# Kernel tuning notes

Measured on AMD Instinct MI355X. Metric: run time of the kernel, lower is better.

The kernel has to match this reference:

```python
import jax, jax.numpy as jnp
import numpy as np


def cheb_mats(N: int, degree: int):
    """Analysis/synthesis Chebyshev matrices, matching torch reference.
    Returns T_pinv [d+1, N], T_eval [N, d+1] as float32 jnp arrays."""
    x = np.linspace(0.0, 1.0, N, dtype=np.float32)
    xn = np.clip(2.0 * x - 1.0, -1 + 1e-06, 1 - 1e-06)
    theta = np.arccos(xn)
    ks = np.arange(degree + 1, dtype=np.float32)
    T = np.cos(theta[:, None] * ks[None, :])  # [N, d+1]
    T_pinv = np.linalg.pinv(T.astype(np.float64)).astype(np.float32)  # [d+1, N]
    return jnp.asarray(T_pinv), jnp.asarray(T.astype(np.float32))


def setup_inputs() -> dict:
    key = jax.random.key(0)
    k1, k2, k3 = jax.random.split(key, 3)
    B, C, H, W = 32, 64, 128, 128
    out_ch, degree = 64, 8
    scale_w = (2.0 / (C * (degree + 1))) ** 0.5
    scale_h = (2.0 / (out_ch * (degree + 1))) ** 0.5
    x = jax.random.normal(k1, (B, C, H, W), dtype=jnp.float32)
    W_w = scale_w * jax.random.normal(k2, (C, out_ch, degree + 1), dtype=jnp.float32)
    W_h = scale_h * jax.random.normal(k3, (out_ch, out_ch, degree + 1), dtype=jnp.float32)
    return {"x": x, "W_w": W_w, "W_h": W_h}


def reference(x, W_w, W_h):
    B, C, H, W = x.shape
    degree = W_w.shape[-1] - 1
    Tp_w, Te_w = cheb_mats(W, degree)  # [k,W], [W,k]
    Tp_h, Te_h = cheb_mats(H, degree)  # [k,H], [H,k]
    # --- mix along width axis with W_w (equivalent to torch's B*H batched 1D) ---
    c = jnp.einsum('bchw,kw->bchk', x, Tp_w)      # analysis: coeffs over width
    m = jnp.einsum('bchk,cok->bohk', c, W_w)      # channel mixing per degree
    y = jnp.einsum('bohk,wk->bohw', m, Te_w)      # synthesis back to width grid
    # --- mix along height axis with W_h ---
    c2 = jnp.einsum('bohw,kh->bokw', y, Tp_h)
    m2 = jnp.einsum('bokw,ofk->bfkw', c2, W_h)
    out = jnp.einsum('bfkw,hk->bfhw', m2, Te_h)   # [B, out_ch, H, W]
    return out
```

## Files before the change

kernel.cpp:

```cpp
#include <hip/hip_runtime.h>
#include <math.h>


#define K9 9

__global__ __launch_bounds__(256) void setup_all(const float* __restrict__ Ww,
                                                 const float* __restrict__ Wh,
                                                 float* __restrict__ Tp,
                                                 float* __restrict__ Te,
                                                 float* __restrict__ Tpt16,
                                                 float* __restrict__ Wt_w,
                                                 float* __restrict__ Wh_f) {
    int tid = threadIdx.x;
    if (blockIdx.x != 0) {
        int gid = (blockIdx.x - 1) * 256 + tid;
        if (gid < 36864) {
            int k = gid / 4096, r = gid % 4096, c = r / 64, o = r % 64;
            Wt_w[gid] = Ww[(c * 64 + o) * 9 + k];
        } else if (gid < 73728) {
            int g = gid - 36864;
            int f = g / 576, r = g % 576, kh = r / 64, o = r % 64;
            Wh_f[g] = Wh[(o * 64 + f) * 9 + kh];
        }
        return;
    }
    __shared__ double Tsh[128 * K9];
    __shared__ double GA[9][18];
    if (tid < 128) {
        int n = tid;
        float xf = (float)((double)n / 127.0);
        float xn = 2.0f * xf - 1.0f;
        const float lo = (float)(-1.0 + 1e-6);
        const float hi = (float)(1.0 - 1e-6);
        xn = fminf(fmaxf(xn, lo), hi);
        float th = acosf(xn);
        for (int k = 0; k < K9; ++k) {
            float tv = cosf(th * (float)k);
            Te[n * K9 + k] = tv;
            Tsh[n * K9 + k] = (double)tv;
        }
    }
    __syncthreads();
    if (tid < 81) {
        int i = tid / 9, j = tid % 9;
        double s = 0.0;
        for (int n = 0; n < 128; ++n) s += Tsh[n * K9 + i] * Tsh[n * K9 + j];
        GA[i][j] = s;
    }
    if (tid >= 81 && tid < 162) {
        int i = (tid - 81) / 9, j = (tid - 81) % 9;
        GA[i][9 + j] = (i == j) ? 1.0 : 0.0;
    }
    __syncthreads();
    int r18 = tid / 18, j18 = tid % 18;
    for (int col = 0; col < 9; ++col) {
        double inv = 0.0;
        if (tid < 18) inv = 1.0 / GA[col][col];
        __syncthreads();
        if (tid < 18) GA[col][tid] *= inv;
        __syncthreads();
        double f = 0.0;
        if (tid < 162 && r18 != col) f = GA[r18][col];
        __syncthreads();
        if (tid < 162 && r18 != col) GA[r18][j18] -= f * GA[col][j18];
        __syncthreads();
    }
    for (int idx = tid; idx < K9 * 128; idx += 256) {
        int k = idx / 128, n = idx % 128;
        double s = 0.0;
        for (int j = 0; j < 9; ++j) s += GA[k][9 + j] * Tsh[n * K9 + j];
        float sv = (float)s;
        Tp[idx] = sv;
        Tpt16[n * 16 + k] = sv;
    }
}

__global__ __launch_bounds__(256, 2) void k1_width(const float* __restrict__ x,
                                                   const float* __restrict__ Wt_w,
                                                   const float* __restrict__ Tpt16,
                                                   const float* __restrict__ Tp,
                                                   float* __restrict__ dpart) {
    __shared__ float xs[64 * 132];
    __shared__ float red[4 * 64 * K9];
    __shared__ float cs[64 * 76];
    int tid = threadIdx.x;
    int b  = blockIdx.x >> 4;
    int h0 = (blockIdx.x & 15) << 3;
    int c   = tid & 63;
    int wid = tid >> 6;
    int qu  = __builtin_amdgcn_readfirstlane(wid);
    const float* tpq = Tpt16 + qu * 512;
    const float* xb = x + (size_t)b * 1048576;

#pragma unroll
    for (int it = 0; it < 8; ++it) {
        int e = it * 256 + tid;
        int cc = e >> 5, w4 = (e & 31) << 2;
        *(float4*)&xs[cc * 132 + w4] =
            *(const float4*)(xb + (size_t)cc * 16384 + (size_t)h0 * 128 + w4);
    }
    __syncthreads();

    float4 pf[8];
    for (int r = 0; r < 8; ++r) {
        if (r < 7) {
#pragma unroll
            for (int it = 0; it < 8; ++it) {
                int e = it * 256 + tid;
                int cc = e >> 5, w4 = (e & 31) << 2;
                pf[it] = *(const float4*)(xb + (size_t)cc * 16384 +
                                          (size_t)(h0 + r + 1) * 128 + w4);
            }
        }
        float acc[K9];
#pragma unroll
        for (int k = 0; k < K9; ++k) acc[k] = 0.f;
        const float* xr = &xs[c * 132 + qu * 32];
#pragma unroll
        for (int w6 = 0; w6 < 8; ++w6) {
            float4 xv = *(const float4*)&xr[w6 * 4];
            const float* tr = tpq + w6 * 64;
#pragma unroll
            for (int k = 0; k < K9; ++k) {
                acc[k] = fmaf(xv.x, tr[k],      acc[k]);
                acc[k] = fmaf(xv.y, tr[16 + k], acc[k]);
                acc[k] = fmaf(xv.z, tr[32 + k], acc[k]);
                acc[k] = fmaf(xv.w, tr[48 + k], acc[k]);
            }
        }
        float* rw = &red[(wid * 64 + c) * K9];
#pragma unroll
        for (int k = 0; k < K9; ++k) rw[k] = acc[k];
        __syncthreads();
        for (int idx = tid; idx < 576; idx += 256) {
            float v = red[idx] + red[576 + idx] + red[1152 + idx] + red[1728 + idx];
            int cc2 = idx / 9, kk = idx - cc2 * 9;
            cs[cc2 * 76 + kk * 8 + r] = v;
        }
        if (r < 7) {
#pragma unroll
            for (int it = 0; it < 8; ++it) {
                int e = it * 256 + tid;
                int cc = e >> 5, w4 = (e & 31) << 2;
                *(float4*)&xs[cc * 132 + w4] = pf[it];
            }
        }
        __syncthreads();
    }

    float* db = dpart + (size_t)blockIdx.x * 5184;
    const float* tph = Tp + h0;
    for (int idx = tid; idx < 576; idx += 256) {
        int o = idx & 63, k = idx >> 6;
        const float* wt = Wt_w + k * 4096 + o;
        float a0 = 0.f, a1 = 0.f, a2 = 0.f, a3 = 0.f;
        float a4 = 0.f, a5 = 0.f, a6 = 0.f, a7 = 0.f;
        for (int cc = 0; cc < 64; ++cc) {
            float wv = wt[cc * 64];
            float4 p0 = *(const float4*)&cs[cc * 76 + k * 8];
            float4 p1 = *(const float4*)&cs[cc * 76 + k * 8 + 4];
            a0 = fmaf(p0.x, wv, a0); a1 = fmaf(p0.y, wv, a1);
            a2 = fmaf(p0.z, wv, a2); a3 = fmaf(p0.w, wv, a3);
            a4 = fmaf(p1.x, wv, a4); a5 = fmaf(p1.y, wv, a5);
            a6 = fmaf(p1.z, wv, a6); a7 = fmaf(p1.w, wv, a7);
        }
#pragma unroll
        for (int kh = 0; kh < K9; ++kh) {
            const float* t = tph + kh * 128;
            float ctr = fmaf(a0, t[0], fmaf(a1, t[1], fmaf(a2, t[2], a3 * t[3])));
            ctr = fmaf(a4, t[4], fmaf(a5, t[5], fmaf(a6, t[6], fmaf(a7, t[7], ctr))));
            db[kh * 576 + idx] = ctr;
        }
    }
}

__global__ __launch_bounds__(256) void k2_reduce(const float* __restrict__ dpart,
                                                 float* __restrict__ d_ws) {
    int gid = blockIdx.x * 256 + threadIdx.x;
    int b = gid / 5184, j = gid - b * 5184;
    const float* p = dpart + (size_t)b * 16 * 5184 + j;
    float s = 0.f;
#pragma unroll
    for (int hg = 0; hg < 16; ++hg) s += p[(size_t)hg * 5184];
    d_ws[gid] = s;
}

__global__ __launch_bounds__(256) void k3_synth(const float* __restrict__ d_ws,
                                                const float* __restrict__ Wh_f,
                                                const float* __restrict__ Te,
                                                float* __restrict__ out) {
    __shared__ float ds[81 * 65];
    __shared__ float whs[9 * 65];
    __shared__ float tes[1152];
    __shared__ float f1[9 * 128];
    __shared__ float el[81];
    int tid = threadIdx.x;
    int bf = blockIdx.x;
    int b = bf >> 6, f = bf & 63;
    const float4* db4 = (const float4*)(d_ws + (size_t)b * 5184);
    for (int i = tid; i < 1296; i += 256) {
        float4 v = db4[i];
        float* dst = &ds[(i >> 4) * 65 + ((i & 15) << 2)];
        dst[0] = v.x; dst[1] = v.y; dst[2] = v.z; dst[3] = v.w;
    }
    const float4* wh4 = (const float4*)(Wh_f + (size_t)f * 576);
    for (int i = tid; i < 144; i += 256) {
        float4 v = wh4[i];
        float* dst = &whs[(i >> 4) * 65 + ((i & 15) << 2)];
        dst[0] = v.x; dst[1] = v.y; dst[2] = v.z; dst[3] = v.w;
    }
    for (int i = tid; i < 288; i += 256) ((float4*)tes)[i] = ((const float4*)Te)[i];
    __syncthreads();
    if (tid < 81) {
        int kh = tid / 9;
        const float* wr = &whs[kh * 65];
        const float* dr = &ds[tid * 65];
        float ea = 0.f;
#pragma unroll 8
        for (int o = 0; o < 64; ++o) ea = fmaf(wr[o], dr[o], ea);
        el[tid] = ea;
    }
    __syncthreads();
    for (int idx = tid; idx < 1152; idx += 256) {
        int kh = idx >> 7, w = idx & 127;
        float acc = 0.f;
#pragma unroll
        for (int kw = 0; kw < 9; ++kw)
            acc = fmaf(el[kh * 9 + kw], tes[w * 9 + kw], acc);
        f1[kh * 128 + w] = acc;
    }
    __syncthreads();
    int w4 = (tid & 31) << 2;
    int hg = tid >> 5;
    float4 fr[9];
#pragma unroll
    for (int k = 0; k < 9; ++k) fr[k] = *(const float4*)&f1[k * 128 + w4];
    float* ob = out + (size_t)bf * 16384;
    for (int h = hg; h < 128; h += 8) {
        const float* th = &tes[h * 9];
        float4 acc = make_float4(0.f, 0.f, 0.f, 0.f);
#pragma unroll
        for (int k = 0; k < 9; ++k) {
            float t = th[k];
            acc.x = fmaf(t, fr[k].x, acc.x);
            acc.y = fmaf(t, fr[k].y, acc.y);
            acc.z = fmaf(t, fr[k].z, acc.z);
            acc.w = fmaf(t, fr[k].w, acc.w);
        }
        *(float4*)(ob + h * 128 + w4) = acc;
    }
}

extern "C" void kernel_launch(void* const* d_in, const int* in_sizes, int n_in,
                              void* d_out, int out_size, void* d_ws, size_t ws_size,
                              hipStream_t stream) {
    (void)in_sizes; (void)n_in; (void)out_size; (void)ws_size;
    const float* x  = (const float*)d_in[0];
    const float* Ww = (const float*)d_in[1];
    const float* Wh = (const float*)d_in[2];
    float* out = (float*)d_out;
    float* ws = (float*)d_ws;
    float* Tp    = ws;
    float* Te    = ws + 1152;
    float* Tpt16 = ws + 2304;
    float* Wt_w  = ws + 4352;
    float* Wh_f  = ws + 41216;
    float* dpart = ws + 78080;
    float* d_d   = ws + 78080 + 2654208;

    setup_all<<<289, 256, 0, stream>>>(Ww, Wh, Tp, Te, Tpt16, Wt_w, Wh_f);
    k1_width<<<512, 256, 0, stream>>>(x, Wt_w, Tpt16, Tp, dpart);
    k2_reduce<<<648, 256, 0, stream>>>(dpart, d_d);
    k3_synth<<<2048, 256, 0, stream>>>(d_d, Wh_f, Te, out);
}
```

Before: 367.4 us.

## Split width kernel into 4-row blocks and drop register prefetch for occupancy

```diff
diff --git a/kernel.cpp b/kernel.cpp
--- a/kernel.cpp
+++ b/kernel.cpp
@@ -75,43 +75,33 @@
     }
 }
 
-__global__ __launch_bounds__(256, 2) void k1_width(const float* __restrict__ x,
+__global__ __launch_bounds__(256, 3) void k1_width(const float* __restrict__ x,
                                                    const float* __restrict__ Wt_w,
                                                    const float* __restrict__ Tpt16,
                                                    const float* __restrict__ Tp,
                                                    float* __restrict__ dpart) {
     __shared__ float xs[64 * 132];
     __shared__ float red[4 * 64 * K9];
-    __shared__ float cs[64 * 76];
+    __shared__ float cs[4 * 64 * K9];
     int tid = threadIdx.x;
-    int b  = blockIdx.x >> 4;
-    int h0 = (blockIdx.x & 15) << 3;
+    int b  = blockIdx.x >> 5;
+    int h0 = (blockIdx.x & 31) << 2;
     int c   = tid & 63;
     int wid = tid >> 6;
     int qu  = __builtin_amdgcn_readfirstlane(wid);
     const float* tpq = Tpt16 + qu * 512;
     const float* xb = x + (size_t)b * 1048576;
 
-#pragma unroll
-    for (int it = 0; it < 8; ++it) {
-        int e = it * 256 + tid;
-        int cc = e >> 5, w4 = (e & 31) << 2;
-        *(float4*)&xs[cc * 132 + w4] =
-            *(const float4*)(xb + (size_t)cc * 16384 + (size_t)h0 * 128 + w4);
-    }
-    __syncthreads();
-
-    float4 pf[8];
-    for (int r = 0; r < 8; ++r) {
-        if (r < 7) {
-#pragma unroll
-            for (int it = 0; it < 8; ++it) {
-                int e = it * 256 + tid;
-                int cc = e >> 5, w4 = (e & 31) << 2;
-                pf[it] = *(const float4*)(xb + (size_t)cc * 16384 +
-                                          (size_t)(h0 + r + 1) * 128 + w4);
-            }
-        }
+    for (int r = 0; r < 4; ++r) {
+#pragma unroll
+        for (int it = 0; it < 8; ++it) {
+            int e = it * 256 + tid;
+            int cc = e >> 5, w4 = (e & 31) << 2;
+            *(float4*)&xs[cc * 132 + w4] =
+                *(const float4*)(xb + (size_t)cc * 16384 +
+                                 (size_t)(h0 + r) * 128 + w4);
+        }
+        __syncthreads();
         float acc[K9];
 #pragma unroll
         for (int k = 0; k < K9; ++k) acc[k] = 0.f;
@@ -134,16 +124,7 @@
         __syncthreads();
         for (int idx = tid; idx < 576; idx += 256) {
             float v = red[idx] + red[576 + idx] + red[1152 + idx] + red[1728 + idx];
-            int cc2 = idx / 9, kk = idx - cc2 * 9;
-            cs[cc2 * 76 + kk * 8 + r] = v;
-        }
-        if (r < 7) {
-#pragma unroll
-            for (int it = 0; it < 8; ++it) {
-                int e = it * 256 + tid;
-                int cc = e >> 5, w4 = (e & 31) << 2;
-                *(float4*)&xs[cc * 132 + w4] = pf[it];
-            }
+            cs[r * 576 + idx] = v;
         }
         __syncthreads();
     }
@@ -154,21 +135,19 @@
         int o = idx & 63, k = idx >> 6;
         const float* wt = Wt_w + k * 4096 + o;
         float a0 = 0.f, a1 = 0.f, a2 = 0.f, a3 = 0.f;
-        float a4 = 0.f, a5 = 0.f, a6 = 0.f, a7 = 0.f;
         for (int cc = 0; cc < 64; ++cc) {
             float wv = wt[cc * 64];
-            float4 p0 = *(const float4*)&cs[cc * 76 + k * 8];
-            float4 p1 = *(const float4*)&cs[cc * 76 + k * 8 + 4];
-            a0 = fmaf(p0.x, wv, a0); a1 = fmaf(p0.y, wv, a1);
-            a2 = fmaf(p0.z, wv, a2); a3 = fmaf(p0.w, wv, a3);
-            a4 = fmaf(p1.x, wv, a4); a5 = fmaf(p1.y, wv, a5);
-            a6 = fmaf(p1.z, wv, a6); a7 = fmaf(p1.w, wv, a7);
+            float i0 = cs[0 * 576 + cc * 9 + k];
+            float i1 = cs[1 * 576 + cc * 9 + k];
+            float i2 = cs[2 * 576 + cc * 9 + k];
+            float i3 = cs[3 * 576 + cc * 9 + k];
+            a0 = fmaf(i0, wv, a0); a1 = fmaf(i1, wv, a1);
+            a2 = fmaf(i2, wv, a2); a3 = fmaf(i3, wv, a3);
         }
 #pragma unroll
         for (int kh = 0; kh < K9; ++kh) {
             const float* t = tph + kh * 128;
             float ctr = fmaf(a0, t[0], fmaf(a1, t[1], fmaf(a2, t[2], a3 * t[3])));
-            ctr = fmaf(a4, t[4], fmaf(a5, t[5], fmaf(a6, t[6], fmaf(a7, t[7], ctr))));
             db[kh * 576 + idx] = ctr;
         }
     }
@@ -178,10 +157,10 @@
                                                  float* __restrict__ d_ws) {
     int gid = blockIdx.x * 256 + threadIdx.x;
     int b = gid / 5184, j = gid - b * 5184;
-    const float* p = dpart + (size_t)b * 16 * 5184 + j;
+    const float* p = dpart + (size_t)b * 32 * 5184 + j;
     float s = 0.f;
 #pragma unroll
-    for (int hg = 0; hg < 16; ++hg) s += p[(size_t)hg * 5184];
+    for (int hg = 0; hg < 32; ++hg) s += p[(size_t)hg * 5184];
     d_ws[gid] = s;
 }
 
@@ -266,10 +245,10 @@
     float* Wt_w  = ws + 4352;
     float* Wh_f  = ws + 41216;
     float* dpart = ws + 78080;
-    float* d_d   = ws + 78080 + 2654208;
+    float* d_d   = ws + 78080 + 5308416;
 
     setup_all<<<289, 256, 0, stream>>>(Ww, Wh, Tp, Te, Tpt16, Wt_w, Wh_f);
-    k1_width<<<512, 256, 0, stream>>>(x, Wt_w, Tpt16, Tp, dpart);
+    k1_width<<<1024, 256, 0, stream>>>(x, Wt_w, Tpt16, Tp, dpart);
     k2_reduce<<<648, 256, 0, stream>>>(dpart, d_d);
     k3_synth<<<2048, 256, 0, stream>>>(d_d, Wh_f, Te, out);
 }
```

New measurement: 325.9 us. 11.3% less time.
